# Optimization experiments

Hardware: AMD Instinct MI355X
Metric: run time of the kernel (lower is better)

## Reference

```python
import jax, jax.numpy as jnp
import numpy as np

B, S, T, E, H, V, L = 128, 128, 8, 300, 512, 50000, 3
G = 4 * H  # LSTM gate dim (i,f,g,o) in torch order


def _lstm_scan(x, Wih, Whh, b):
    # x: [B, S, E] -> h outputs [B, S, H]; torch gate order i,f,g,o
    Bq = x.shape[0]
    Hq = Whh.shape[1]
    def step(carry, xt):
        h, c = carry
        g = xt @ Wih.T + h @ Whh.T + b
        i, f, gg, o = jnp.split(g, 4, axis=-1)
        c = jax.nn.sigmoid(f) * c + jax.nn.sigmoid(i) * jnp.tanh(gg)
        h = jax.nn.sigmoid(o) * jnp.tanh(c)
        return (h, c), h
    h0 = jnp.zeros((Bq, Hq), x.dtype)
    _, ys = jax.lax.scan(step, (h0, h0), jnp.swapaxes(x, 0, 1))
    return jnp.swapaxes(ys, 0, 1)


def _bilstm(x, lengths, Wih_f, Whh_f, b_f, Wih_b, Whh_b, b_b):
    # Packed-sequence BiLSTM: backward pass runs over length-aware reversed
    # tokens; outputs zero-padded beyond each sequence length.
    Sq = x.shape[1]
    t = jnp.arange(Sq)[None, :]
    Ln = lengths[:, None]
    out_f = _lstm_scan(x, Wih_f, Whh_f, b_f)
    idx = jnp.where(t < Ln, Ln - 1 - t, t)
    x_rev = jnp.take_along_axis(x, idx[:, :, None], axis=1)
    out_b = _lstm_scan(x_rev, Wih_b, Whh_b, b_b)
    out_b = jnp.take_along_axis(out_b, idx[:, :, None], axis=1)
    out = jnp.concatenate([out_f, out_b], axis=-1)
    return out * (t < Ln)[:, :, None].astype(out.dtype)


def setup_inputs() -> dict:
    key = jax.random.key(0)
    ks = jax.random.split(key, 24)
    rn = lambda k, shp: jax.random.normal(k, shp, jnp.float32) * 0.05
    return {
        "raw_text": jax.random.randint(ks[0], (B, S), 1, V),
        "target": jax.random.randint(ks[1], (B, T), 1, V),
        "target_span": jnp.sort(jax.random.randint(ks[2], (B, 2), 0, S), axis=1),
        "label": jax.random.randint(ks[3], (B,), 0, L),
        "emb_W": rn(ks[4], (V, E)),
        "l1f_Wih": rn(ks[5], (G, E)), "l1f_Whh": rn(ks[6], (G, H)), "l1f_b": rn(ks[7], (G,)),
        "l1b_Wih": rn(ks[8], (G, E)), "l1b_Whh": rn(ks[9], (G, H)), "l1b_b": rn(ks[10], (G,)),
        "l2f_Wih": rn(ks[11], (G, E)), "l2f_Whh": rn(ks[12], (G, H)), "l2f_b": rn(ks[13], (G,)),
        "l2b_Wih": rn(ks[14], (G, E)), "l2b_Whh": rn(ks[15], (G, H)), "l2b_b": rn(ks[16], (G,)),
        "conv_w": rn(ks[17], (50, 2 * H, 3)), "conv_b": rn(ks[18], (50,)),
        "fc1_w": rn(ks[19], (2 * H, 4 * H)), "fc1_b": rn(ks[20], (2 * H,)),
        "fc_w": rn(ks[21], (L, 50)), "fc_b": rn(ks[22], (L,)),
    }


def reference(raw_text, target, target_span, label, emb_W,
              l1f_Wih, l1f_Whh, l1f_b, l1b_Wih, l1b_Whh, l1b_b,
              l2f_Wih, l2f_Whh, l2f_b, l2b_Wih, l2b_Whh, l2b_b,
              conv_w, conv_b, fc1_w, fc1_b, fc_w, fc_b):
    feature_len = jnp.sum(raw_text != 0, axis=-1)
    aspect_len = jnp.sum(target != 0, axis=-1)
    feature = emb_W[raw_text]   # [B, S, E]
    aspect = emb_W[target]      # [B, T, E]
    v = _bilstm(feature, feature_len, l1f_Wih, l1f_Whh, l1f_b, l1b_Wih, l1b_Whh, l1b_b)  # [B,S,2H]
    e = _bilstm(aspect, aspect_len, l2f_Wih, l2f_Whh, l2f_b, l2b_Wih, l2b_Whh, l2b_b)    # [B,T,2H]
    v = jnp.swapaxes(v, 1, 2)  # [B, 2H, S]
    e = jnp.swapaxes(e, 1, 2)  # [B, 2H, T]
    # vectorized position weights (replaces per-batch CPU loop)
    j = jnp.arange(S)[None, :]
    p0 = target_span[:, 0:1]
    p1 = target_span[:, 1:2]
    w = jnp.where(j < p1,
                  1.0 - (p1 - j).astype(v.dtype) / 40.0,
                  1.0 - (j - p0).astype(v.dtype) / 40.0)  # [B, S]
    for _ in range(2):
        a = jax.nn.softmax(jnp.einsum('bct,bcs->bts', e, v), axis=1)  # softmax over aspect dim
        mid = jnp.einsum('bct,bts->bcs', e, a)                         # [B, 2H, S]
        mid = jnp.concatenate([mid, v], axis=1)                        # [B, 4H, S]
        mid = jax.nn.relu(jnp.einsum('bcs,oc->bos', mid, fc1_w) + fc1_b[None, :, None])
        v = (mid + v) * w[:, None, :]
    z = jax.lax.conv_general_dilated(v, conv_w, (1,), [(1, 1)],
                                     dimension_numbers=('NCW', 'OIW', 'NCW'))
    z = jax.nn.relu(z + conv_b[None, :, None])
    z = jnp.max(z, axis=2)          # max_pool1d over full length, squeeze
    logits = z @ fc_w.T + fc_b      # [B, L]
    logp = jax.nn.log_softmax(logits, axis=-1)
    loss = -jnp.mean(jnp.take_along_axis(logp, label[:, None], axis=1))
    return (loss, logits)
```

## Files before the change

### kernel.cpp

```cpp
#include <hip/hip_runtime.h>
#include <hip/hip_bf16.h>
#include <math.h>

#define Bn 128
#define Sn 128
#define Tn 8
#define En 300
#define EnP 320
#define Hn 512
#define Gn 2048
#define C2n 1024
#define NCONV 50
#define CH 16
#define NCH 8

typedef unsigned short ushort_t;
typedef __attribute__((ext_vector_type(8))) short bf16x8;
typedef __attribute__((ext_vector_type(4))) float f32x4;
typedef __attribute__((ext_vector_type(8))) unsigned short ushort8_t;

#define OFF_X1C   0L
#define OFF_X2    4194304L
#define OFF_FEATP 6291456L
#define OFF_ASPP  8912896L
#define OFF_WIHI  9076736L
#define OFF_BIASI 10387456L
#define OFF_FC1WB 10395648L
#define OFF_CWT   11444224L
#define OFF_V     11597824L
#define OFF_E     19986432L
#define OFF_F2    20510720L
#define OFF_STATE 21035008L
#define OFF_LENF  21559296L
#define OFF_LENA  21559424L
#define OFF_RMF1  21559552L
#define OFF_RMB1  21575936L
#define OFF_RM2   21592320L
#define OFF_WPOS  21593344L
#define OFF_ZPART 21609728L
#define WS_NEED_F 21635328L
#define OFF_MO    0L

__device__ __forceinline__ float sigm_(float x){ return 1.f/(1.f + __expf(-x)); }
__device__ __forceinline__ float tanh_(float x){ return 2.f/(1.f + __expf(-2.f*x)) - 1.f; }
__device__ __forceinline__ float bfu2f(ushort_t u){ return __uint_as_float(((unsigned int)u) << 16); }
__device__ __forceinline__ ushort_t f2bfu(float f){
    __hip_bfloat16 h = __float2bfloat16(f);
    return *reinterpret_cast<ushort_t*>(&h);
}
__device__ __forceinline__ void gload16(const void* g, void* l){
    __builtin_amdgcn_global_load_lds(
        (const __attribute__((address_space(1))) void*)g,
        (__attribute__((address_space(3))) void*)l, 16, 0, 0);
}

__global__ void zero_kernel(float* __restrict__ p, long n){
    long i = (long)blockIdx.x*256 + threadIdx.x;
    if (i < n) p[i] = 0.f;
}

__global__ __launch_bounds__(128) void prep_kernel(
    const int* __restrict__ raw_text, const int* __restrict__ target,
    const int* __restrict__ span,
    int* __restrict__ lenf, int* __restrict__ lena,
    int* __restrict__ rmF1, int* __restrict__ rmB1, int* __restrict__ rm2,
    float* __restrict__ wpos)
{
    int b = blockIdx.x, tid = threadIdx.x;
    __shared__ int sh[128];
    sh[tid] = (raw_text[b*Sn + tid] != 0) ? 1 : 0;
    __syncthreads();
    for (int off = 64; off > 0; off >>= 1){
        if (tid < off) sh[tid] += sh[tid + off];
        __syncthreads();
    }
    __shared__ int lfs, las;
    if (tid == 0){
        lfs = sh[0]; lenf[b] = lfs;
        int c = 0;
        for (int tt = 0; tt < Tn; tt++) c += (target[b*Tn + tt] != 0) ? 1 : 0;
        las = c; lena[b] = c;
    }
    __syncthreads();
    int Lf = lfs, La = las;
    int t = tid;
    int c = t >> 4, tt = t & 15;
    int rev = (t < Lf) ? (Lf - 1 - t) : t;
    rmF1[(c*Bn + b)*CH + tt] = b*Sn + t;
    rmB1[(c*Bn + b)*CH + tt] = b*Sn + rev;
    if (t < Tn) rm2[b*Tn + t] = b*Tn + ((t < La) ? (La - 1 - t) : t);
    float p0 = (float)span[b*2 + 0], p1 = (float)span[b*2 + 1];
    float j = (float)t;
    wpos[b*Sn + t] = (j < p1) ? (1.0f - (p1 - j)/40.0f) : (1.0f - (j - p0)/40.0f);
}

__global__ void embed_kernel(const int* __restrict__ ids, const float* __restrict__ embW,
                             ushort_t* __restrict__ out, long rows)
{
    long i = (long)blockIdx.x*256 + threadIdx.x;
    if (i >= rows*EnP) return;
    long r = i / EnP; int c = (int)(i - r*EnP);
    out[i] = (c < En) ? f2bfu(embW[(long)ids[r]*En + c]) : (ushort_t)0;
}

__global__ void cvtpad_inter(const float* __restrict__ src, ushort_t* __restrict__ dst){
    long i = (long)blockIdx.x*256 + threadIdx.x;
    if (i >= (long)Gn*EnP) return;
    int jr = (int)(i / EnP), c = (int)(i - (long)jr*EnP);
    dst[i] = (c < En) ? f2bfu(src[(long)((jr&3)*Hn + (jr>>2))*En + c]) : (ushort_t)0;
}

__global__ void bias_inter(const float* __restrict__ src, float* __restrict__ dst){
    int i = blockIdx.x*256 + threadIdx.x;
    if (i >= Gn) return;
    dst[i] = src[(i&3)*Hn + (i>>2)];
}

__global__ void cvtpad_kernel(const float* __restrict__ src, ushort_t* __restrict__ dst,
                              int rows, int K, int Kp)
{
    long i = (long)blockIdx.x*256 + threadIdx.x;
    if (i >= (long)rows*Kp) return;
    int r = (int)(i / Kp), c = (int)(i - (long)r*Kp);
    dst[i] = (c < K) ? f2bfu(src[(long)r*K + c]) : (ushort_t)0;
}

__global__ void convw_kernel(const float* __restrict__ cw, float* __restrict__ cwT){
    int i = blockIdx.x*256 + threadIdx.x;
    if (i >= NCONV*3*1024) return;
    int o = i / 3072, rem = i % 3072, k = rem / 1024, c = rem % 1024;
    cwT[i] = cw[o*3072 + c*3 + k];
}

__global__ __launch_bounds__(256) void mfma_gemm(
    const ushort_t* __restrict__ A, int lda, const int* __restrict__ rowmap,
    const ushort_t* __restrict__ Wb, int ldw, const float* __restrict__ bias,
    ushort_t* __restrict__ C, int ldc, int M, int N, int K)
{
    __shared__ ushort_t As[128*32];
    __shared__ ushort_t Bs[128*32];
    int tid = threadIdx.x;
    int lane = tid & 63, wid = tid >> 6;
    int m0 = blockIdx.y * 128, n0 = blockIdx.x * 128;
    int wr = wid >> 1, wc = wid & 1;

    int ms0 = tid >> 2, ch0 = tid & 3;
    int arow0 = m0 + ms0, arow1 = m0 + ms0 + 64;
    if (rowmap){ arow0 = rowmap[arow0]; arow1 = rowmap[arow1]; }
    const ushort_t* Aptr0 = A + (long)arow0*lda;
    const ushort_t* Aptr1 = A + (long)arow1*lda;
    const ushort_t* Bptr0 = Wb + (long)(n0 + ms0)*ldw;
    const ushort_t* Bptr1 = Wb + (long)(n0 + ms0 + 64)*ldw;
    int swk = (ch0 ^ ((ms0 >> 1) & 3)) * 8;

    ushort_t* AsB0 = As + wid*512;
    ushort_t* AsB1 = As + 2048 + wid*512;
    ushort_t* BsB0 = Bs + wid*512;
    ushort_t* BsB1 = Bs + 2048 + wid*512;

    f32x4 acc[4][4];
    #pragma unroll
    for (int i = 0; i < 4; i++)
        #pragma unroll
        for (int j = 0; j < 4; j++) acc[i][j] = (f32x4){0.f, 0.f, 0.f, 0.f};

    int r = lane & 15, g = lane >> 4;
    for (int kt = 0; kt < K; kt += 32){
        gload16(Aptr0 + kt + swk, AsB0);
        gload16(Aptr1 + kt + swk, AsB1);
        gload16(Bptr0 + kt + swk, BsB0);
        gload16(Bptr1 + kt + swk, BsB1);
        __syncthreads();
        bf16x8 af[4], bw[4];
        #pragma unroll
        for (int i = 0; i < 4; i++){
            int msA = wr*64 + i*16 + r;
            af[i] = *(const bf16x8*)(As + msA*32 + ((g ^ ((msA >> 1) & 3)) * 8));
            int msB = wc*64 + i*16 + r;
            bw[i] = *(const bf16x8*)(Bs + msB*32 + ((g ^ ((msB >> 1) & 3)) * 8));
        }
        #pragma unroll
        for (int i = 0; i < 4; i++)
            #pragma unroll
            for (int j = 0; j < 4; j++)
                acc[i][j] = __builtin_amdgcn_mfma_f32_16x16x32_bf16(af[i], bw[j], acc[i][j], 0, 0, 0);
        __syncthreads();
    }
    #pragma unroll
    for (int i = 0; i < 4; i++){
        int row = m0 + wr*64 + i*16 + g*4;
        #pragma unroll
        for (int j = 0; j < 4; j++){
            int col = n0 + wc*64 + j*16 + r;
            float bv = bias ? bias[col] : 0.f;
            #pragma unroll
            for (int q = 0; q < 4; q++)
                C[(long)(row + q)*ldc + col] = f2bfu(acc[i][j][q] + bv);
        }
    }
}

__global__ __launch_bounds__(256) void lstm_step2(
    const float* __restrict__ WhF, const float* __restrict__ WhB,
    const ushort_t* __restrict__ Xf, const ushort_t* __restrict__ Xb,
    const ushort_t* __restrict__ hprev, ushort_t* __restrict__ hnext,
    float* __restrict__ cst, ushort_t* __restrict__ out,
    const int* __restrict__ lens, int t, int tloc, int Pout, int CHin)
{
    int dir = blockIdx.y;
    const float* Wh = dir ? WhB : WhF;
    const ushort_t* X = dir ? Xb : Xf;
    const ushort_t* hp = hprev + dir*65536;
    ushort_t* hn = hnext + dir*65536;
    float* cc = cst + dir*65536;
    int j0 = blockIdx.x * 16;
    int tid = threadIdx.x, lane = tid & 63, wv = tid >> 6;
    int r15 = lane & 15, kg = lane >> 4;

    __shared__ ushort_t Ws[64*512];
    __shared__ ushort_t Hs[128*32];

    #pragma unroll
    for (int it = 0; it < 16; it++){
        int id = it*256 + tid;
        int row = id >> 6, ch = id & 63;
        const float* src = Wh + (long)((row&3)*Hn + j0 + (row>>2))*Hn + ch*8;
        float4 f0 = *(const float4*)src;
        float4 f1 = *(const float4*)(src + 4);
        ushort8_t w8;
        w8[0]=f2bfu(f0.x); w8[1]=f2bfu(f0.y); w8[2]=f2bfu(f0.z); w8[3]=f2bfu(f0.w);
        w8[4]=f2bfu(f1.x); w8[5]=f2bfu(f1.y); w8[6]=f2bfu(f1.z); w8[7]=f2bfu(f1.w);
        *(ushort8_t*)(Ws + row*512 + ((ch ^ (row&7))*8)) = w8;
    }

    f32x4 acc[4][2];
    #pragma unroll
    for (int i = 0; i < 4; i++){ acc[i][0] = (f32x4){0.f,0.f,0.f,0.f}; acc[i][1] = (f32x4){0.f,0.f,0.f,0.f}; }

    int sb = tid >> 2, sc = (tid & 3)*8;
    for (int kt = 0; kt < 16; kt++){
        gload16(hp + sb*512 + kt*32 + sc,        Hs + wv*512);
        gload16(hp + (64+sb)*512 + kt*32 + sc,   Hs + 2048 + wv*512);
        __syncthreads();
        bf16x8 af[4], bfr[2];
        #pragma unroll
        for (int i = 0; i < 4; i++){
            int row = i*16 + r15;
            af[i] = *(const bf16x8*)(Ws + row*512 + (((kt*4 + kg) ^ (row&7))*8));
        }
        #pragma unroll
        for (int jc = 0; jc < 2; jc++){
            int b = wv*32 + jc*16 + r15;
            bfr[jc] = *(const bf16x8*)(Hs + b*32 + kg*8);
        }
        #pragma unroll
        for (int i = 0; i < 4; i++)
            #pragma unroll
            for (int jc = 0; jc < 2; jc++)
                acc[i][jc] = __builtin_amdgcn_mfma_f32_16x16x32_bf16(af[i], bfr[jc], acc[i][jc], 0, 0, 0);
        __syncthreads();
    }

    #pragma unroll
    for (int i = 0; i < 4; i++){
        int rowq = i*16 + kg*4;
        int j = j0 + (rowq >> 2);
        #pragma unroll
        for (int jc = 0; jc < 2; jc++){
            int b = wv*32 + jc*16 + r15;
            int len = lens[b];
            ushort4 xg = *(const ushort4*)(X + (((long)(b*CHin + tloc)) << 11) + (j0 << 2) + rowq);
            float gi = acc[i][jc][0] + bfu2f(xg.x);
            float gf = acc[i][jc][1] + bfu2f(xg.y);
            float gg = acc[i][jc][2] + bfu2f(xg.z);
            float go = acc[i][jc][3] + bfu2f(xg.w);
            int ci = b*Hn + j;
            float cn = sigm_(gf)*cc[ci] + sigm_(gi)*tanh_(gg);
            cc[ci] = cn;
            float hv = sigm_(go)*tanh_(cn);
            hn[ci] = f2bfu(hv);
            int pos = dir ? ((t < len) ? (len - 1 - t) : t) : t;
            out[((long)b*Pout + pos)*C2n + dir*Hn + j] = (t < len) ? f2bfu(hv) : (ushort_t)0;
        }
    }
}

__global__ __launch_bounds__(256) void attn2_kernel(
    ushort_t* __restrict__ v, const ushort_t* __restrict__ e,
    const ushort_t* __restrict__ F2, const ushort_t* __restrict__ mo,
    const float* __restrict__ fc1_b, const float* __restrict__ wpos)
{
    int s = blockIdx.x, b = blockIdx.y;
    ushort_t* vrow = v + ((long)b*Sn + s)*C2n;
    const ushort_t* eb = e + (long)b*Tn*C2n;
    const ushort_t* Fb = F2 + (long)b*Tn*C2n;
    const ushort_t* morow = mo + ((long)b*Sn + s)*C2n;
    int c0 = threadIdx.x * 4;

    ushort4 vv4 = *(const ushort4*)(vrow + c0);
    float v0 = bfu2f(vv4.x), v1 = bfu2f(vv4.y), v2 = bfu2f(vv4.z), v3 = bfu2f(vv4.w);

    float part[8];
    #pragma unroll
    for (int tt = 0; tt < 8; tt++){
        ushort4 ee = *(const ushort4*)(eb + tt*C2n + c0);
        part[tt] = v0*bfu2f(ee.x) + v1*bfu2f(ee.y) + v2*bfu2f(ee.z) + v3*bfu2f(ee.w);
    }
    __shared__ float red[8][4];
    int lane = threadIdx.x & 63, wid = threadIdx.x >> 6;
    #pragma unroll
    for (int tt = 0; tt < 8; tt++){
        float x = part[tt];
        for (int off = 32; off > 0; off >>= 1) x += __shfl_down(x, off);
        if (lane == 0) red[tt][wid] = x;
    }
    __syncthreads();
    float a[8]; float mx = -1e30f, sum = 0.f;
    #pragma unroll
    for (int tt = 0; tt < 8; tt++){
        float sv = red[tt][0] + red[tt][1] + red[tt][2] + red[tt][3];
        a[tt] = sv; mx = fmaxf(mx, sv);
    }
    #pragma unroll
    for (int tt = 0; tt < 8; tt++){ a[tt] = __expf(a[tt] - mx); sum += a[tt]; }
    float inv = 1.f / sum;
    #pragma unroll
    for (int tt = 0; tt < 8; tt++) a[tt] *= inv;

    float m0f = 0.f, m1f = 0.f, m2f = 0.f, m3f = 0.f;
    #pragma unroll
    for (int tt = 0; tt < 8; tt++){
        ushort4 ff = *(const ushort4*)(Fb + tt*C2n + c0);
        m0f += a[tt]*bfu2f(ff.x); m1f += a[tt]*bfu2f(ff.y);
        m2f += a[tt]*bfu2f(ff.z); m3f += a[tt]*bfu2f(ff.w);
    }
    ushort4 mm = *(const ushort4*)(morow + c0);
    float w = wpos[b*Sn + s];
    float o0 = (fmaxf(m0f + bfu2f(mm.x) + fc1_b[c0+0], 0.f) + v0) * w;
    float o1 = (fmaxf(m1f + bfu2f(mm.y) + fc1_b[c0+1], 0.f) + v1) * w;
    float o2 = (fmaxf(m2f + bfu2f(mm.z) + fc1_b[c0+2], 0.f) + v2) * w;
    float o3 = (fmaxf(m3f + bfu2f(mm.w) + fc1_b[c0+3], 0.f) + v3) * w;
    ushort4 outv;
    outv.x = f2bfu(o0); outv.y = f2bfu(o1); outv.z = f2bfu(o2); outv.w = f2bfu(o3);
    *(ushort4*)(vrow + c0) = outv;
}

__global__ __launch_bounds__(256) void conv2_kernel(
    const ushort_t* __restrict__ v, const float* __restrict__ cwT,
    const float* __restrict__ cb, float* __restrict__ zpart)
{
    int st = blockIdx.x, b = blockIdx.y;
    int s0 = st * 32;
    __shared__ ushort_t vs[34*1024];
    for (int i = threadIdx.x; i < 34*128; i += 256){
        int rr = i >> 7, ck = i & 127;
        int ss = s0 - 1 + rr;
        ushort8_t val = {0,0,0,0,0,0,0,0};
        if (ss >= 0 && ss < Sn) val = *(const ushort8_t*)(v + ((long)b*Sn + ss)*C2n + ck*8);
        *(ushort8_t*)(vs + rr*1024 + ((ck ^ (rr&7))*8)) = val;
    }
    __syncthreads();
    int sl = threadIdx.x & 31, ob = threadIdx.x >> 5;
    for (int o = ob; o < NCONV; o += 8){
        float acc = cb[o];
        #pragma unroll
        for (int k = 0; k < 3; k++){
            int row = sl + k;
            const ushort_t* vrow = vs + row*1024;
            int rsw = row & 7;
            const float* wrow = cwT + (o*3 + k)*1024;
            float a0 = 0.f;
            for (int c8 = 0; c8 < 128; c8++){
                ushort8_t vv = *(const ushort8_t*)(vrow + ((c8 ^ rsw)*8));
                const float* wp = wrow + c8*8;
                float4 wa = *(const float4*)(wp);
                float4 wb = *(const float4*)(wp + 4);
                a0 += bfu2f(vv[0])*wa.x + bfu2f(vv[1])*wa.y + bfu2f(vv[2])*wa.z + bfu2f(vv[3])*wa.w
                    + bfu2f(vv[4])*wb.x + bfu2f(vv[5])*wb.y + bfu2f(vv[6])*wb.z + bfu2f(vv[7])*wb.w;
            }
            acc += a0;
        }
        float rv = fmaxf(acc, 0.f);
        for (int off = 16; off > 0; off >>= 1) rv = fmaxf(rv, __shfl_down(rv, off));
        if (sl == 0) zpart[((long)b*NCONV + o)*4 + st] = rv;
    }
}

__global__ __launch_bounds__(128) void loss_kernel(
    const float* __restrict__ zpart, const float* __restrict__ fcw,
    const float* __restrict__ fcb, const int* __restrict__ label,
    float* __restrict__ out)
{
    int b = threadIdx.x;
    float lg0 = fcb[0], lg1 = fcb[1], lg2 = fcb[2];
    for (int k = 0; k < NCONV; k++){
        const float* zp = zpart + ((long)b*NCONV + k)*4;
        float zm = fmaxf(fmaxf(zp[0], zp[1]), fmaxf(zp[2], zp[3]));
        lg0 += zm * fcw[k];
        lg1 += zm * fcw[NCONV + k];
        lg2 += zm * fcw[2*NCONV + k];
    }
    out[1 + b*3 + 0] = lg0;
    out[1 + b*3 + 1] = lg1;
    out[1 + b*3 + 2] = lg2;
    float mx = fmaxf(lg0, fmaxf(lg1, lg2));
    float sum = expf(lg0-mx) + expf(lg1-mx) + expf(lg2-mx);
    float lse = mx + logf(sum);
    int lb = label[b];
    float lp = ((lb == 0) ? lg0 : (lb == 1) ? lg1 : lg2) - lse;
    __shared__ float red[128];
    red[b] = lp; __syncthreads();
    for (int off = 64; off > 0; off >>= 1){
        if (b < off) red[b] += red[b + off];
        __syncthreads();
    }
    if (b == 0) out[0] = -red[0] / (float)Bn;
}

extern "C" void kernel_launch(void* const* d_in, const int* in_sizes, int n_in,
                              void* d_out, int out_size, void* d_ws, size_t ws_size,
                              hipStream_t stream)
{
    (void)in_sizes; (void)n_in; (void)out_size;
    if (ws_size < (size_t)WS_NEED_F * 4) return;
    const int* raw_text  = (const int*)d_in[0];
    const int* target    = (const int*)d_in[1];
    const int* span      = (const int*)d_in[2];
    const int* label     = (const int*)d_in[3];
    const float* embW    = (const float*)d_in[4];
    const float* l1f_Wih = (const float*)d_in[5];
    const float* l1f_Whh = (const float*)d_in[6];
    const float* l1f_b   = (const float*)d_in[7];
    const float* l1b_Wih = (const float*)d_in[8];
    const float* l1b_Whh = (const float*)d_in[9];
    const float* l1b_b   = (const float*)d_in[10];
    const float* l2f_Wih = (const float*)d_in[11];
    const float* l2f_Whh = (const float*)d_in[12];
    const float* l2f_b   = (const float*)d_in[13];
    const float* l2b_Wih = (const float*)d_in[14];
    const float* l2b_Whh = (const float*)d_in[15];
    const float* l2b_b   = (const float*)d_in[16];
    const float* conv_w  = (const float*)d_in[17];
    const float* conv_b  = (const float*)d_in[18];
    const float* fc1_w   = (const float*)d_in[19];
    const float* fc1_b   = (const float*)d_in[20];
    const float* fc_w    = (const float*)d_in[21];
    const float* fc_b    = (const float*)d_in[22];

    float* ws = (float*)d_ws;
    ushort_t* Xf1   = (ushort_t*)(ws + OFF_X1C);
    ushort_t* Xb1   = Xf1 + 4194304;
    ushort_t* Xf2   = (ushort_t*)(ws + OFF_X2);
    ushort_t* Xb2   = Xf2 + 2097152;
    ushort_t* featp = (ushort_t*)(ws + OFF_FEATP);
    ushort_t* aspp  = (ushort_t*)(ws + OFF_ASPP);
    ushort_t* WihI  = (ushort_t*)(ws + OFF_WIHI);
    float*    biasI = ws + OFF_BIASI;
    ushort_t* fc1wb = (ushort_t*)(ws + OFF_FC1WB);
    float*    cwT   = ws + OFF_CWT;
    ushort_t* vbuf  = (ushort_t*)(ws + OFF_V);
    ushort_t* ebuf  = (ushort_t*)(ws + OFF_E);
    ushort_t* F2b   = (ushort_t*)(ws + OFF_F2);
    ushort_t* mo    = (ushort_t*)(ws + OFF_MO);
    float* st   = ws + OFF_STATE;
    int* lenf   = (int*)(ws + OFF_LENF);
    int* lena   = (int*)(ws + OFF_LENA);
    int* rmF1   = (int*)(ws + OFF_RMF1);
    int* rmB1   = (int*)(ws + OFF_RMB1);
    int* rm2    = (int*)(ws + OFF_RM2);
    float* wpos = ws + OFF_WPOS;
    float* zpart= ws + OFF_ZPART;

    ushort_t* h1A = (ushort_t*)(st);
    ushort_t* h1B = (ushort_t*)(st + 65536);
    float*    c1  = st + 131072;
    float* st2 = st + 262144;
    ushort_t* h2A = (ushort_t*)(st2);
    ushort_t* h2B = (ushort_t*)(st2 + 65536);
    float*    c2  = st2 + 131072;

    zero_kernel<<<2048, 256, 0, stream>>>(st, 524288L);
    prep_kernel<<<Bn, 128, 0, stream>>>(raw_text, target, span, lenf, lena, rmF1, rmB1, rm2, wpos);
    embed_kernel<<<(Bn*Sn*EnP + 255)/256, 256, 0, stream>>>(raw_text, embW, featp, (long)Bn*Sn);
    embed_kernel<<<(Bn*Tn*EnP + 255)/256, 256, 0, stream>>>(target, embW, aspp, (long)Bn*Tn);

    const float* wih_src[4]  = {l1f_Wih, l1b_Wih, l2f_Wih, l2b_Wih};
    const float* bias_src[4] = {l1f_b,   l1b_b,   l2f_b,   l2b_b};
    for (int d = 0; d < 4; d++){
        cvtpad_inter<<<(Gn*EnP + 255)/256, 256, 0, stream>>>(wih_src[d], WihI + (long)d*655360);
        bias_inter<<<8, 256, 0, stream>>>(bias_src[d], biasI + d*2048);
    }
    cvtpad_kernel<<<(1024*2048 + 255)/256, 256, 0, stream>>>(fc1_w, fc1wb, 1024, 2048, 2048);
    convw_kernel<<<(NCONV*3072 + 255)/256, 256, 0, stream>>>(conv_w, cwT);

    dim3 gc(Gn/128, (Bn*CH)/128);
    dim3 gl(32, 2);
    for (int c = 0; c < NCH; c++){
        mfma_gemm<<<gc, 256, 0, stream>>>(featp, EnP, rmF1 + c*Bn*CH, WihI,            EnP, biasI,        Xf1, Gn, Bn*CH, Gn, EnP);
        mfma_gemm<<<gc, 256, 0, stream>>>(featp, EnP, rmB1 + c*Bn*CH, WihI + 655360,   EnP, biasI + 2048, Xb1, Gn, Bn*CH, Gn, EnP);
        for (int tt = 0; tt < CH; tt++){
            int t = c*CH + tt;
            const ushort_t* hpv = (t & 1) ? h1B : h1A;
            ushort_t*       hnv = (t & 1) ? h1A : h1B;
            lstm_step2<<<gl, 256, 0, stream>>>(l1f_Whh, l1b_Whh, Xf1, Xb1,
                hpv, hnv, c1, vbuf, lenf, t, tt, Sn, CH);
        }
    }
    dim3 g2(Gn/128, (Bn*Tn)/128);
    mfma_gemm<<<g2, 256, 0, stream>>>(aspp, EnP, nullptr, WihI + 2L*655360, EnP, biasI + 4096, Xf2, Gn, Bn*Tn, Gn, EnP);
    mfma_gemm<<<g2, 256, 0, stream>>>(aspp, EnP, rm2,     WihI + 3L*655360, EnP, biasI + 6144, Xb2, Gn, Bn*Tn, Gn, EnP);
    for (int t = 0; t < Tn; t++){
        const ushort_t* hpv = (t & 1) ? h2B : h2A;
        ushort_t*       hnv = (t & 1) ? h2A : h2B;
        lstm_step2<<<gl, 256, 0, stream>>>(l2f_Whh, l2b_Whh, Xf2, Xb2,
            hpv, hnv, c2, ebuf, lena, t, t, Tn, Tn);
    }

    dim3 gF(C2n/128, (Bn*Tn)/128);
    mfma_gemm<<<gF, 256, 0, stream>>>(ebuf, C2n, nullptr, fc1wb, 2048, nullptr, F2b, C2n, Bn*Tn, C2n, C2n);

    dim3 gm(C2n/128, (Bn*Sn)/128);
    for (int it = 0; it < 2; it++){
        mfma_gemm<<<gm, 256, 0, stream>>>(vbuf, C2n, nullptr, fc1wb + 1024, 2048, nullptr, mo, C2n, Bn*Sn, C2n, C2n);
        attn2_kernel<<<dim3(Sn, Bn), 256, 0, stream>>>(vbuf, ebuf, F2b, mo, fc1_b, wpos);
    }

    conv2_kernel<<<dim3(4, Bn), 256, 0, stream>>>(vbuf, cwT, conv_b, zpart);
    loss_kernel<<<1, 128, 0, stream>>>(zpart, fc_w, fc_b, label, (float*)d_out);
}
```

Baseline: 2.848 ms.

## Replace per-step LSTM launches with persistent kernel using grid barrier and fused input projection

The per-timestep lstm_step2 launches and the chunked input-projection GEMMs are replaced by one persistent kernel per LSTM layer. Each block keeps its slices of Whh and Wih in LDS and computes the input projection inline from gathered embedding rows. Blocks synchronise across timesteps with an atomic-counter grid barrier instead of kernel boundaries. This removes launch overhead and the precomputed X buffers, but adds spin-barrier cost, reads h directly from global memory without LDS staging, and depends on all 64 blocks being co-resident.

Measured after the change: 3.873 ms. 36.0% more time.

```diff
diff --git a/kernel.cpp b/kernel.cpp
--- a/kernel.cpp
+++ b/kernel.cpp
@@ -11,35 +11,34 @@
 #define Gn 2048
 #define C2n 1024
 #define NCONV 50
-#define CH 16
-#define NCH 8
 
 typedef unsigned short ushort_t;
 typedef __attribute__((ext_vector_type(8))) short bf16x8;
 typedef __attribute__((ext_vector_type(4))) float f32x4;
 typedef __attribute__((ext_vector_type(8))) unsigned short ushort8_t;
 
-#define OFF_X1C   0L
-#define OFF_X2    4194304L
-#define OFF_FEATP 6291456L
-#define OFF_ASPP  8912896L
-#define OFF_WIHI  9076736L
-#define OFF_BIASI 10387456L
-#define OFF_FC1WB 10395648L
-#define OFF_CWT   11444224L
-#define OFF_V     11597824L
-#define OFF_E     19986432L
-#define OFF_F2    20510720L
-#define OFF_STATE 21035008L
-#define OFF_LENF  21559296L
-#define OFF_LENA  21559424L
-#define OFF_RMF1  21559552L
-#define OFF_RMB1  21575936L
-#define OFF_RM2   21592320L
-#define OFF_WPOS  21593344L
-#define OFF_ZPART 21609728L
-#define WS_NEED_F 21635328L
-#define OFF_MO    0L
+#define OFF_V      0L
+#define OFF_E      8388608L
+#define OFF_F2     8912896L
+#define OFF_FC1WB  9437184L
+#define OFF_CWT    10485760L
+#define OFF_STATE  10639360L
+#define OFF_SYNC   11163648L
+#define OFF_RMF1T  11163904L
+#define OFF_RMB1T  11180288L
+#define OFF_RM2FT  11196672L
+#define OFF_RM2BT  11197696L
+#define OFF_LENF   11198720L
+#define OFF_LENA   11198848L
+#define OFF_WPOS   11198976L
+#define OFF_ZPART  11215360L
+#define OFF_UNION  11240960L
+#define OFF_FEATP  OFF_UNION
+#define OFF_ASPP   (OFF_UNION + 2621440L)
+#define OFF_WIHI   (OFF_UNION + 2785280L)
+#define OFF_BIASI  (OFF_UNION + 4096000L)
+#define OFF_MO     OFF_UNION
+#define WS_NEED_F  19629568L
 
 __device__ __forceinline__ float sigm_(float x){ return 1.f/(1.f + __expf(-x)); }
 __device__ __forceinline__ float tanh_(float x){ return 2.f/(1.f + __expf(-2.f*x)) - 1.f; }
@@ -63,7 +62,8 @@
     const int* __restrict__ raw_text, const int* __restrict__ target,
     const int* __restrict__ span,
     int* __restrict__ lenf, int* __restrict__ lena,
-    int* __restrict__ rmF1, int* __restrict__ rmB1, int* __restrict__ rm2,
+    int* __restrict__ rmF1t, int* __restrict__ rmB1t,
+    int* __restrict__ rm2Ft, int* __restrict__ rm2Bt,
     float* __restrict__ wpos)
 {
     int b = blockIdx.x, tid = threadIdx.x;
@@ -84,11 +84,13 @@
     __syncthreads();
     int Lf = lfs, La = las;
     int t = tid;
-    int c = t >> 4, tt = t & 15;
     int rev = (t < Lf) ? (Lf - 1 - t) : t;
-    rmF1[(c*Bn + b)*CH + tt] = b*Sn + t;
-    rmB1[(c*Bn + b)*CH + tt] = b*Sn + rev;
-    if (t < Tn) rm2[b*Tn + t] = b*Tn + ((t < La) ? (La - 1 - t) : t);
+    rmF1t[t*Bn + b] = b*Sn + t;
+    rmB1t[t*Bn + b] = b*Sn + rev;
+    if (t < Tn){
+        rm2Ft[t*Bn + b] = b*Tn + t;
+        rm2Bt[t*Bn + b] = b*Tn + ((t < La) ? (La - 1 - t) : t);
+    }
     float p0 = (float)span[b*2 + 0], p1 = (float)span[b*2 + 1];
     float j = (float)t;
     wpos[b*Sn + t] = (j < p1) ? (1.0f - (p1 - j)/40.0f) : (1.0f - (j - p0)/40.0f);
@@ -200,25 +202,31 @@
     }
 }
 
-__global__ __launch_bounds__(256) void lstm_step2(
+__global__ __launch_bounds__(256) void lstm_persist(
     const float* __restrict__ WhF, const float* __restrict__ WhB,
-    const ushort_t* __restrict__ Xf, const ushort_t* __restrict__ Xb,
-    const ushort_t* __restrict__ hprev, ushort_t* __restrict__ hnext,
+    const ushort_t* __restrict__ WihBase, long wihDirStride,
+    const float* __restrict__ biasBase,
+    const ushort_t* __restrict__ feat,
+    const int* __restrict__ rmF, const int* __restrict__ rmB,
+    ushort_t* __restrict__ hA, ushort_t* __restrict__ hB,
     float* __restrict__ cst, ushort_t* __restrict__ out,
-    const int* __restrict__ lens, int t, int tloc, int Pout, int CHin)
+    const int* __restrict__ lens, int P, int Pout,
+    unsigned* __restrict__ sync_cnt)
 {
     int dir = blockIdx.y;
     const float* Wh = dir ? WhB : WhF;
-    const ushort_t* X = dir ? Xb : Xf;
-    const ushort_t* hp = hprev + dir*65536;
-    ushort_t* hn = hnext + dir*65536;
+    const ushort_t* Wx = WihBase + (long)dir*wihDirStride;
+    const float* bias = biasBase + dir*2048;
+    const int* rm = dir ? rmB : rmF;
+    ushort_t* hbufA = hA + dir*65536;
+    ushort_t* hbufB = hB + dir*65536;
     float* cc = cst + dir*65536;
     int j0 = blockIdx.x * 16;
     int tid = threadIdx.x, lane = tid & 63, wv = tid >> 6;
     int r15 = lane & 15, kg = lane >> 4;
 
-    __shared__ ushort_t Ws[64*512];
-    __shared__ ushort_t Hs[128*32];
+    __shared__ ushort_t WsH[64*512];
+    __shared__ ushort_t WsX[64*EnP];
 
     #pragma unroll
     for (int it = 0; it < 16; it++){
@@ -230,58 +238,102 @@
         ushort8_t w8;
         w8[0]=f2bfu(f0.x); w8[1]=f2bfu(f0.y); w8[2]=f2bfu(f0.z); w8[3]=f2bfu(f0.w);
         w8[4]=f2bfu(f1.x); w8[5]=f2bfu(f1.y); w8[6]=f2bfu(f1.z); w8[7]=f2bfu(f1.w);
-        *(ushort8_t*)(Ws + row*512 + ((ch ^ (row&7))*8)) = w8;
-    }
-
-    f32x4 acc[4][2];
-    #pragma unroll
-    for (int i = 0; i < 4; i++){ acc[i][0] = (f32x4){0.f,0.f,0.f,0.f}; acc[i][1] = (f32x4){0.f,0.f,0.f,0.f}; }
-
-    int sb = tid >> 2, sc = (tid & 3)*8;
-    for (int kt = 0; kt < 16; kt++){
-        gload16(hp + sb*512 + kt*32 + sc,        Hs + wv*512);
-        gload16(hp + (64+sb)*512 + kt*32 + sc,   Hs + 2048 + wv*512);
+        *(ushort8_t*)(WsH + row*512 + ((ch ^ (row&7))*8)) = w8;
+    }
+    #pragma unroll
+    for (int it = 0; it < 10; it++){
+        int id = it*256 + tid;
+        int row = id / 40, ch = id - row*40;
+        ushort8_t w8 = *(const ushort8_t*)(Wx + (long)(j0*4 + row)*EnP + ch*8);
+        *(ushort8_t*)(WsX + row*EnP + ((ch ^ (row&7))*8)) = w8;
+    }
+    __syncthreads();
+
+    int bidx[2], lenv[2];
+    #pragma unroll
+    for (int jc = 0; jc < 2; jc++){
+        bidx[jc] = wv*32 + jc*16 + r15;
+        lenv[jc] = lens[bidx[jc]];
+    }
+
+    const ushort_t* hp = hbufA;
+    ushort_t* hn = hbufB;
+    for (int t = 0; t < P; ++t){
+        int xrow[2];
+        #pragma unroll
+        for (int jc = 0; jc < 2; jc++) xrow[jc] = rm[t*Bn + bidx[jc]];
+
+        f32x4 acc[4][2];
+        #pragma unroll
+        for (int i = 0; i < 4; i++){
+            acc[i][0] = (f32x4){0.f,0.f,0.f,0.f};
+            acc[i][1] = (f32x4){0.f,0.f,0.f,0.f};
+        }
+        #pragma unroll
+        for (int kt = 0; kt < 16; kt++){
+            bf16x8 af[4], bh[2];
+            #pragma unroll
+            for (int i = 0; i < 4; i++){
+                int row = i*16 + r15;
+                af[i] = *(const bf16x8*)(WsH + row*512 + (((kt*4 + kg) ^ (row&7))*8));
+            }
+            #pragma unroll
+            for (int jc = 0; jc < 2; jc++)
+                bh[jc] = *(const bf16x8*)(hp + bidx[jc]*512 + kt*32 + kg*8);
+            #pragma unroll
+            for (int i = 0; i < 4; i++)
+                #pragma unroll
+                for (int jc = 0; jc < 2; jc++)
+                    acc[i][jc] = __builtin_amdgcn_mfma_f32_16x16x32_bf16(af[i], bh[jc], acc[i][jc], 0, 0, 0);
+        }
+        #pragma unroll
+        for (int kt = 0; kt < 10; kt++){
+            bf16x8 ax[4], bx[2];
+            #pragma unroll
+            for (int i = 0; i < 4; i++){
+                int row = i*16 + r15;
+                ax[i] = *(const bf16x8*)(WsX + row*EnP + (((kt*4 + kg) ^ (row&7))*8));
+            }
+            #pragma unroll
+            for (int jc = 0; jc < 2; jc++)
+                bx[jc] = *(const bf16x8*)(feat + (long)xrow[jc]*EnP + kt*32 + kg*8);
+            #pragma unroll
+            for (int i = 0; i < 4; i++)
+                #pragma unroll
+                for (int jc = 0; jc < 2; jc++)
+                    acc[i][jc] = __builtin_amdgcn_mfma_f32_16x16x32_bf16(ax[i], bx[jc], acc[i][jc], 0, 0, 0);
+        }
+        #pragma unroll
+        for (int i = 0; i < 4; i++){
+            int rowq = i*16 + kg*4;
+            int j = j0 + (rowq >> 2);
+            float4 b4 = *(const float4*)(bias + j0*4 + rowq);
+            #pragma unroll
+            for (int jc = 0; jc < 2; jc++){
+                int b = bidx[jc], len = lenv[jc];
+                float gi = acc[i][jc][0] + b4.x;
+                float gf = acc[i][jc][1] + b4.y;
+                float gg = acc[i][jc][2] + b4.z;
+                float go = acc[i][jc][3] + b4.w;
+                int ci = b*Hn + j;
+                float cn = sigm_(gf)*cc[ci] + sigm_(gi)*tanh_(gg);
+                cc[ci] = cn;
+                float hv = sigm_(go)*tanh_(cn);
+                hn[ci] = f2bfu(hv);
+                int pos = dir ? ((t < len) ? (len - 1 - t) : t) : t;
+                out[((long)b*Pout + pos)*C2n + dir*Hn + j] = (t < len) ? f2bfu(hv) : (ushort_t)0;
+            }
+        }
+        __threadfence();
         __syncthreads();
-        bf16x8 af[4], bfr[2];
-        #pragma unroll
-        for (int i = 0; i < 4; i++){
-            int row = i*16 + r15;
-            af[i] = *(const bf16x8*)(Ws + row*512 + (((kt*4 + kg) ^ (row&7))*8));
-        }
-        #pragma unroll
-        for (int jc = 0; jc < 2; jc++){
-            int b = wv*32 + jc*16 + r15;
-            bfr[jc] = *(const bf16x8*)(Hs + b*32 + kg*8);
-        }
-        #pragma unroll
-        for (int i = 0; i < 4; i++)
-            #pragma unroll
-            for (int jc = 0; jc < 2; jc++)
-                acc[i][jc] = __builtin_amdgcn_mfma_f32_16x16x32_bf16(af[i], bfr[jc], acc[i][jc], 0, 0, 0);
+        if (tid == 0){
+            atomicAdd(sync_cnt, 1u);
+            unsigned tgt = 64u * (unsigned)(t + 1);
+            while (atomicAdd(sync_cnt, 0u) < tgt) __builtin_amdgcn_s_sleep(1);
+        }
         __syncthreads();
-    }
-
-    #pragma unroll
-    for (int i = 0; i < 4; i++){
-        int rowq = i*16 + kg*4;
-        int j = j0 + (rowq >> 2);
-        #pragma unroll
-        for (int jc = 0; jc < 2; jc++){
-            int b = wv*32 + jc*16 + r15;
-            int len = lens[b];
-            ushort4 xg = *(const ushort4*)(X + (((long)(b*CHin + tloc)) << 11) + (j0 << 2) + rowq);
-            float gi = acc[i][jc][0] + bfu2f(xg.x);
-            float gf = acc[i][jc][1] + bfu2f(xg.y);
-            float gg = acc[i][jc][2] + bfu2f(xg.z);
-            float go = acc[i][jc][3] + bfu2f(xg.w);
-            int ci = b*Hn + j;
-            float cn = sigm_(gf)*cc[ci] + sigm_(gi)*tanh_(gg);
-            cc[ci] = cn;
-            float hv = sigm_(go)*tanh_(cn);
-            hn[ci] = f2bfu(hv);
-            int pos = dir ? ((t < len) ? (len - 1 - t) : t) : t;
-            out[((long)b*Pout + pos)*C2n + dir*Hn + j] = (t < len) ? f2bfu(hv) : (ushort_t)0;
-        }
+        __threadfence();
+        const ushort_t* tmp = hp; hp = hn; hn = (ushort_t*)tmp;
     }
 }
 
@@ -448,28 +500,26 @@
     const float* fc_b    = (const float*)d_in[22];
 
     float* ws = (float*)d_ws;
-    ushort_t* Xf1   = (ushort_t*)(ws + OFF_X1C);
-    ushort_t* Xb1   = Xf1 + 4194304;
-    ushort_t* Xf2   = (ushort_t*)(ws + OFF_X2);
-    ushort_t* Xb2   = Xf2 + 2097152;
+    ushort_t* vbuf  = (ushort_t*)(ws + OFF_V);
+    ushort_t* ebuf  = (ushort_t*)(ws + OFF_E);
+    ushort_t* F2b   = (ushort_t*)(ws + OFF_F2);
+    ushort_t* fc1wb = (ushort_t*)(ws + OFF_FC1WB);
+    float*    cwT   = ws + OFF_CWT;
+    float*    st    = ws + OFF_STATE;
+    unsigned* sync  = (unsigned*)(ws + OFF_SYNC);
+    int* rmF1t = (int*)(ws + OFF_RMF1T);
+    int* rmB1t = (int*)(ws + OFF_RMB1T);
+    int* rm2Ft = (int*)(ws + OFF_RM2FT);
+    int* rm2Bt = (int*)(ws + OFF_RM2BT);
+    int* lenf  = (int*)(ws + OFF_LENF);
+    int* lena  = (int*)(ws + OFF_LENA);
+    float* wpos = ws + OFF_WPOS;
+    float* zpart= ws + OFF_ZPART;
     ushort_t* featp = (ushort_t*)(ws + OFF_FEATP);
     ushort_t* aspp  = (ushort_t*)(ws + OFF_ASPP);
     ushort_t* WihI  = (ushort_t*)(ws + OFF_WIHI);
     float*    biasI = ws + OFF_BIASI;
-    ushort_t* fc1wb = (ushort_t*)(ws + OFF_FC1WB);
-    float*    cwT   = ws + OFF_CWT;
-    ushort_t* vbuf  = (ushort_t*)(ws + OFF_V);
-    ushort_t* ebuf  = (ushort_t*)(ws + OFF_E);
-    ushort_t* F2b   = (ushort_t*)(ws + OFF_F2);
     ushort_t* mo    = (ushort_t*)(ws + OFF_MO);
-    float* st   = ws + OFF_STATE;
-    int* lenf   = (int*)(ws + OFF_LENF);
-    int* lena   = (int*)(ws + OFF_LENA);
-    int* rmF1   = (int*)(ws + OFF_RMF1);
-    int* rmB1   = (int*)(ws + OFF_RMB1);
-    int* rm2    = (int*)(ws + OFF_RM2);
-    float* wpos = ws + OFF_WPOS;
-    float* zpart= ws + OFF_ZPART;
 
     ushort_t* h1A = (ushort_t*)(st);
     ushort_t* h1B = (ushort_t*)(st + 65536);
@@ -479,8 +529,9 @@
     ushort_t* h2B = (ushort_t*)(st2 + 65536);
     float*    c2  = st2 + 131072;
 
-    zero_kernel<<<2048, 256, 0, stream>>>(st, 524288L);
-    prep_kernel<<<Bn, 128, 0, stream>>>(raw_text, target, span, lenf, lena, rmF1, rmB1, rm2, wpos);
+    zero_kernel<<<2049, 256, 0, stream>>>(st, 524288L + 256L);
+    prep_kernel<<<Bn, 128, 0, stream>>>(raw_text, target, span, lenf, lena,
+                                        rmF1t, rmB1t, rm2Ft, rm2Bt, wpos);
     embed_kernel<<<(Bn*Sn*EnP + 255)/256, 256, 0, stream>>>(raw_text, embW, featp, (long)Bn*Sn);
     embed_kernel<<<(Bn*Tn*EnP + 255)/256, 256, 0, stream>>>(target, embW, aspp, (long)Bn*Tn);
 
@@ -493,28 +544,11 @@
     cvtpad_kernel<<<(1024*2048 + 255)/256, 256, 0, stream>>>(fc1_w, fc1wb, 1024, 2048, 2048);
     convw_kernel<<<(NCONV*3072 + 255)/256, 256, 0, stream>>>(conv_w, cwT);
 
-    dim3 gc(Gn/128, (Bn*CH)/128);
     dim3 gl(32, 2);
-    for (int c = 0; c < NCH; c++){
-        mfma_gemm<<<gc, 256, 0, stream>>>(featp, EnP, rmF1 + c*Bn*CH, WihI,            EnP, biasI,        Xf1, Gn, Bn*CH, Gn, EnP);
-        mfma_gemm<<<gc, 256, 0, stream>>>(featp, EnP, rmB1 + c*Bn*CH, WihI + 655360,   EnP, biasI + 2048, Xb1, Gn, Bn*CH, Gn, EnP);
-        for (int tt = 0; tt < CH; tt++){
-            int t = c*CH + tt;
-            const ushort_t* hpv = (t & 1) ? h1B : h1A;
-            ushort_t*       hnv = (t & 1) ? h1A : h1B;
-            lstm_step2<<<gl, 256, 0, stream>>>(l1f_Whh, l1b_Whh, Xf1, Xb1,
-                hpv, hnv, c1, vbuf, lenf, t, tt, Sn, CH);
-        }
-    }
-    dim3 g2(Gn/128, (Bn*Tn)/128);
-    mfma_gemm<<<g2, 256, 0, stream>>>(aspp, EnP, nullptr, WihI + 2L*655360, EnP, biasI + 4096, Xf2, Gn, Bn*Tn, Gn, EnP);
-    mfma_gemm<<<g2, 256, 0, stream>>>(aspp, EnP, rm2,     WihI + 3L*655360, EnP, biasI + 6144, Xb2, Gn, Bn*Tn, Gn, EnP);
-    for (int t = 0; t < Tn; t++){
-        const ushort_t* hpv = (t & 1) ? h2B : h2A;
-        ushort_t*       hnv = (t & 1) ? h2A : h2B;
-        lstm_step2<<<gl, 256, 0, stream>>>(l2f_Whh, l2b_Whh, Xf2, Xb2,
-            hpv, hnv, c2, ebuf, lena, t, t, Tn, Tn);
-    }
+    lstm_persist<<<gl, 256, 0, stream>>>(l1f_Whh, l1b_Whh, WihI, 655360L, biasI,
+        featp, rmF1t, rmB1t, h1A, h1B, c1, vbuf, lenf, Sn, Sn, sync);
+    lstm_persist<<<gl, 256, 0, stream>>>(l2f_Whh, l2b_Whh, WihI + 2L*655360, 655360L, biasI + 4096,
+        aspp, rm2Ft, rm2Bt, h2A, h2B, c2, ebuf, lena, Tn, Tn, sync + 32);
 
     dim3 gF(C2n/128, (Bn*Tn)/128);
     mfma_gemm<<<gF, 256, 0, stream>>>(ebuf, C2n, nullptr, fc1wb, 2048, nullptr, F2b, C2n, Bn*Tn, C2n, C2n);
```
